# Optimization experiments

Hardware: AMD Instinct MI355X
Metric: run time of the kernel (lower is better)

Reference implementation:

```python
import jax, jax.numpy as jnp
import numpy as np

N_NODES = 100000
N_EDGES = 1600000
D_FEAT = 64


def setup_inputs() -> dict:
    key = jax.random.key(0)
    k1, k2 = jax.random.split(key)
    x = jax.random.normal(k1, (N_NODES, D_FEAT), dtype=jnp.float32)
    edge_index = jax.random.randint(k2, (2, N_EDGES), 0, N_NODES, dtype=jnp.int64)
    alpha = jnp.ones((), dtype=jnp.float32)
    res_scale = jnp.ones((), dtype=jnp.float32)
    return {"x": x, "alpha": alpha, "res_scale": res_scale, "edge_index": edge_index}


def reference(x, alpha, res_scale, edge_index):
    """LGConv (symmetric gcn_norm, no self-loops) -> alpha-scale -> residual.

    out_i = alpha * sum_{(j->i) in E} x_j / sqrt(deg_i * deg_j) + res_scale * x_i
    """
    n = x.shape[0]
    row, col = edge_index[0], edge_index[1]  # source, target
    # degree from target index (as in PyG gcn_norm with add_self_loops=False)
    deg = jax.ops.segment_sum(jnp.ones(row.shape[0], dtype=x.dtype), col, num_segments=n)
    deg_inv_sqrt = jnp.where(deg > 0, jax.lax.rsqrt(jnp.maximum(deg, 1.0)), 0.0)
    norm = deg_inv_sqrt[row] * deg_inv_sqrt[col]  # (E,)
    msgs = norm[:, None] * x[row]                  # (E, d) gather + scale
    out = jax.ops.segment_sum(msgs, col, num_segments=n)  # scatter-add to targets
    return alpha * out + res_scale * x
```

## Files before the change

kernel.cpp:

```cpp
#include <hip/hip_runtime.h>
#include <hip/hip_bf16.h>

#define D_FEAT 64
#define OVF_CAP 65536
#define EB 4096
#define NBMAX 1024

typedef unsigned int uint32;

__device__ inline float blo(uint32 u) { return __uint_as_float(u << 16); }
__device__ inline float bhi(uint32 u) { return __uint_as_float(u & 0xffff0000u); }
__device__ inline float dinv(int d) { return (d > 0) ? rsqrtf((float)d) : 0.0f; }

__global__ __launch_bounds__(1024) void k_scatter(const int* __restrict__ row,
                                                  const int* __restrict__ col,
                                                  const float2* __restrict__ x2,
                                                  uint32* __restrict__ xb,
                                                  int* __restrict__ deg,
                                                  int* __restrict__ cursor,
                                                  uint32* __restrict__ binned,
                                                  int* __restrict__ slots,
                                                  int2* __restrict__ ovf,
                                                  int* __restrict__ ovf_cnt,
                                                  int nhalf, int E, int nb,
                                                  int CAP, int C) {
    __shared__ int h[NBMAX];
    for (int i = threadIdx.x; i < nb; i += 1024) h[i] = 0;
    __syncthreads();
    const int s = blockIdx.x * EB;
    const int e = (s + EB < E) ? s + EB : E;
    for (int i = s + threadIdx.x; i < e; i += 1024)
        atomicAdd(&h[col[i] >> 7], 1);
    __syncthreads();
    for (int k = threadIdx.x; k < nb; k += 1024) {
        int c = h[k];
        if (c) h[k] = atomicAdd(&cursor[k], c);
    }
    __syncthreads();
    for (int i = s + threadIdx.x; i < e; i += 1024) {
        int c = col[i];
        uint32 r = (uint32)row[i];
        int b = c >> 7;
        int pos = atomicAdd(&h[b], 1);
        if (pos < CAP) {
            binned[(size_t)b * CAP + pos] = (r << 7) | (uint32)(c & 127);
        } else {
            int rk = atomicAdd(&deg[c], 1);
            if (rk < C) {
                slots[(size_t)c * C + rk] = (int)r;
            } else {
                int o = atomicAdd(ovf_cnt, 1);
                if (o < OVF_CAP) ovf[o] = make_int2((int)r, c);
            }
        }
    }
    const int t = blockIdx.x * 1024 + threadIdx.x;
    const int stride = gridDim.x * 1024;
    for (int j = t; j < nhalf; j += stride) {
        float2 v = x2[j];
        __hip_bfloat16 bx = __float2bfloat16(v.x);
        __hip_bfloat16 by = __float2bfloat16(v.y);
        uint32 ux = *reinterpret_cast<unsigned short*>(&bx);
        uint32 uy = *reinterpret_cast<unsigned short*>(&by);
        xb[j] = ux | (uy << 16);
    }
}

__global__ __launch_bounds__(512) void k_build(const int* __restrict__ cursor,
                                               const uint32* __restrict__ binned,
                                               int* __restrict__ slots,
                                               int* __restrict__ deg,
                                               float* __restrict__ winv,
                                               int2* __restrict__ ovf,
                                               int* __restrict__ ovf_cnt,
                                               int n, int C, int CAP) {
    __shared__ int cnt[128];
    const int k = blockIdx.x;
    const int base = k << 7;
    if (threadIdx.x < 128) {
        int node = base + threadIdx.x;
        cnt[threadIdx.x] = (node < n) ? deg[node] : 0;
    }
    __syncthreads();
    int tot = cursor[k];
    const int e = (tot < CAP) ? tot : CAP;
    const uint32* seg = binned + (size_t)k * CAP;
    for (int i = threadIdx.x; i < e; i += 512) {
        uint32 pk = seg[i];
        int cl = (int)(pk & 127);
        int r  = (int)(pk >> 7);
        int rk = atomicAdd(&cnt[cl], 1);
        if (rk < C) {
            slots[(size_t)(base + cl) * C + rk] = r;
        } else {
            int o = atomicAdd(ovf_cnt, 1);
            if (o < OVF_CAP) ovf[o] = make_int2(r, base + cl);
        }
    }
    __syncthreads();
    int i = base + threadIdx.x;
    if (threadIdx.x < 128 && i < n) {
        int d = cnt[threadIdx.x];
        deg[i] = d;
        winv[i] = dinv(d);
    }
}

__global__ void k_gather4d(const uint32* __restrict__ xb,
                           const float4* __restrict__ x4,
                           const int* __restrict__ deg,
                           const float* __restrict__ winv,
                           const int* __restrict__ slots,
                           const float* __restrict__ alpha_p,
                           const float* __restrict__ rs_p,
                           float4* __restrict__ out4, int n, int C) {
    int wid = (blockIdx.x * blockDim.x + threadIdx.x) >> 6;
    if (wid >= n) return;
    const int lane = threadIdx.x & 63;
    const int q = lane >> 4;
    const int l = lane & 15;
    int d = deg[wid];
    int e = (d < C) ? d : C;
    float4 xr = make_float4(0.f, 0.f, 0.f, 0.f);
    if (q == 0) xr = x4[(size_t)wid * 16 + l];
    const int* sl = slots + (size_t)wid * C;
    float ax = 0.f, ay = 0.f, az = 0.f, aw = 0.f;
    int k = 0;
    for (; k + 16 <= e; k += 16) {
        int s0 = sl[k + q];
        int s1 = sl[k + 4 + q];
        int s2 = sl[k + 8 + q];
        int s3 = sl[k + 12 + q];
        float w0 = winv[s0], w1 = winv[s1], w2 = winv[s2], w3 = winv[s3];
        uint2 p0 = ((const uint2*)(xb + (size_t)s0 * 32))[l];
        uint2 p1 = ((const uint2*)(xb + (size_t)s1 * 32))[l];
        uint2 p2 = ((const uint2*)(xb + (size_t)s2 * 32))[l];
        uint2 p3 = ((const uint2*)(xb + (size_t)s3 * 32))[l];
        ax = fmaf(w0, blo(p0.x), ax); ay = fmaf(w0, bhi(p0.x), ay);
        az = fmaf(w0, blo(p0.y), az); aw = fmaf(w0, bhi(p0.y), aw);
        ax = fmaf(w1, blo(p1.x), ax); ay = fmaf(w1, bhi(p1.x), ay);
        az = fmaf(w1, blo(p1.y), az); aw = fmaf(w1, bhi(p1.y), aw);
        ax = fmaf(w2, blo(p2.x), ax); ay = fmaf(w2, bhi(p2.x), ay);
        az = fmaf(w2, blo(p2.y), az); aw = fmaf(w2, bhi(p2.y), aw);
        ax = fmaf(w3, blo(p3.x), ax); ay = fmaf(w3, bhi(p3.x), ay);
        az = fmaf(w3, blo(p3.y), az); aw = fmaf(w3, bhi(p3.y), aw);
    }
    for (; k < e; k += 4) {
        int kk = k + q;
        if (kk < e) {
            int s0 = sl[kk];
            float w0 = winv[s0];
            uint2 p0 = ((const uint2*)(xb + (size_t)s0 * 32))[l];
            ax = fmaf(w0, blo(p0.x), ax); ay = fmaf(w0, bhi(p0.x), ay);
            az = fmaf(w0, blo(p0.y), az); aw = fmaf(w0, bhi(p0.y), aw);
        }
    }
    ax += __shfl_down(ax, 32, 64); ay += __shfl_down(ay, 32, 64);
    az += __shfl_down(az, 32, 64); aw += __shfl_down(aw, 32, 64);
    ax += __shfl_down(ax, 16, 64); ay += __shfl_down(ay, 16, 64);
    az += __shfl_down(az, 16, 64); aw += __shfl_down(aw, 16, 64);
    if (q == 0) {
        float adw = (*alpha_p) * winv[wid];
        float rs  = *rs_p;
        float4 o;
        o.x = fmaf(adw, ax, rs * xr.x);
        o.y = fmaf(adw, ay, rs * xr.y);
        o.z = fmaf(adw, az, rs * xr.z);
        o.w = fmaf(adw, aw, rs * xr.w);
        out4[(size_t)wid * 16 + l] = o;
    }
}

__global__ void k_ovf(const int2* __restrict__ ovf, const int* __restrict__ cnt_p,
                      const float* __restrict__ x, const float* __restrict__ winv,
                      const float* __restrict__ alpha_p, float* __restrict__ out) {
    int cnt = *cnt_p;
    if (cnt > OVF_CAP) cnt = OVF_CAP;
    if (cnt <= 0) return;
    float a = *alpha_p;
    long long total = (long long)cnt * 64;
    long long stride = (long long)gridDim.x * blockDim.x;
    for (long long idx = blockIdx.x * (long long)blockDim.x + threadIdx.x;
         idx < total; idx += stride) {
        int e = (int)(idx >> 6);
        int f = (int)(idx & 63);
        int2 rc = ovf[e];
        float w = a * winv[rc.x] * winv[rc.y];
        atomicAdd(&out[(size_t)rc.y * D_FEAT + f], w * x[(size_t)rc.x * D_FEAT + f]);
    }
}

__global__ void k_winv(const int* __restrict__ deg, float* __restrict__ winv, int n) {
    int i = blockIdx.x * blockDim.x + threadIdx.x;
    if (i < n) winv[i] = dinv(deg[i]);
}

__global__ __launch_bounds__(256) void k_prep(const float2* __restrict__ x2,
                                              uint32* __restrict__ xb,
                                              const int* __restrict__ row,
                                              const int* __restrict__ col,
                                              int* __restrict__ deg,
                                              int* __restrict__ slots,
                                              int2* __restrict__ ovf,
                                              int* __restrict__ ovf_cnt,
                                              int nhalf, int E, int C) {
    const int t = blockIdx.x * blockDim.x + threadIdx.x;
    if (t < E) {
        int c = col[t];
        int r = row[t];
        int rk = atomicAdd(&deg[c], 1);
        if (rk < C) {
            slots[(size_t)c * C + rk] = r;
        } else {
            int o = atomicAdd(ovf_cnt, 1);
            if (o < OVF_CAP) ovf[o] = make_int2(r, c);
        }
    }
    const int stride = gridDim.x * blockDim.x;
    for (int j = t; j < nhalf; j += stride) {
        float2 v = x2[j];
        __hip_bfloat16 bx = __float2bfloat16(v.x);
        __hip_bfloat16 by = __float2bfloat16(v.y);
        uint32 ux = *reinterpret_cast<unsigned short*>(&bx);
        uint32 uy = *reinterpret_cast<unsigned short*>(&by);
        xb[j] = ux | (uy << 16);
    }
}

static inline char* align_up(char* p, size_t a) {
    return (char*)(((uintptr_t)p + (a - 1)) & ~(uintptr_t)(a - 1));
}

extern "C" void kernel_launch(void* const* d_in, const int* in_sizes, int n_in,
                              void* d_out, int out_size, void* d_ws, size_t ws_size,
                              hipStream_t stream) {
    const float* x         = (const float*)d_in[0];
    const float* alpha     = (const float*)d_in[1];
    const float* res_scale = (const float*)d_in[2];
    const int*   ei        = (const int*)d_in[3];

    const int n = in_sizes[0] / D_FEAT;
    const int E = in_sizes[3] / 2;
    const int* row = ei;
    const int* col = ei + E;

    float* out = (float*)d_out;
    const int nhalf = n * (D_FEAT / 2);
    const int nb = (n + 127) >> 7;
    const int B  = (E + EB - 1) / EB;
    const int C  = 32;

    {
        char* p = (char*)d_ws;
        int*    deg     = (int*)p;            p += (size_t)n * 4;
        int*    cursor  = (int*)p;            p += (size_t)nb * 4;
        int*    ovf_cnt = (int*)p;            p += 4;
        float*  winv    = (float*)p;          p += (size_t)n * 4;
        int2*   ovf     = (int2*)p;           p += (size_t)OVF_CAP * 8;
        p = align_up(p, 16);
        uint32* xb      = (uint32*)p;         p += (size_t)n * 128;
        int*    slots   = (int*)p;            p += (size_t)n * C * 4;
        p = align_up(p, 16);
        uint32* binned  = (uint32*)p;
        const size_t fixed = (size_t)((char*)binned - (char*)d_ws);

        int CAP = 0;
        if (ws_size > fixed) {
            long long avail = (long long)(ws_size - fixed) / ((long long)nb * 4);
            CAP = (avail > 4096) ? 4096 : (int)avail;
            CAP &= ~31;
        }
        const bool ok = (CAP >= 1600) && (nb <= NBMAX) && (n <= (NBMAX << 7));
        if (ok) {
            hipMemsetAsync(deg, 0, (size_t)(n + nb + 1) * 4, stream);
            k_scatter<<<B, 1024, 0, stream>>>(row, col, (const float2*)x, xb,
                                              deg, cursor, binned, slots,
                                              ovf, ovf_cnt, nhalf, E, nb, CAP, C);
            k_build<<<nb, 512, 0, stream>>>(cursor, binned, slots, deg, winv,
                                            ovf, ovf_cnt, n, C, CAP);
            const long long tt = (long long)n * D_FEAT;
            const int blocks = (int)((tt + 255) / 256);
            k_gather4d<<<blocks, 256, 0, stream>>>(xb, (const float4*)x, deg, winv,
                                                   slots, alpha, res_scale,
                                                   (float4*)out, n, C);
            k_ovf<<<64, 256, 0, stream>>>(ovf, ovf_cnt, x, winv, alpha, out);
            return;
        }
    }

    {
        char* q = (char*)d_ws;
        int*    degf    = (int*)q;            q += (size_t)n * 4;
        int*    ovf_cf  = (int*)q;            q += 4;
        float*  winvf   = (float*)q;          q += (size_t)n * 4;
        int2*   ovff    = (int2*)q;           q += (size_t)OVF_CAP * 8;
        q = align_up(q, 16);
        uint32* xbf     = (uint32*)q;         q += (size_t)n * 128;
        int*    slotsf  = (int*)q;
        const size_t fxd = (size_t)(q - (char*)d_ws);
        int Cf = 0;
        if (ws_size > fxd) {
            size_t c_avail = (ws_size - fxd) / ((size_t)n * 4);
            Cf = (c_avail > 32) ? 32 : (int)c_avail;
        }
        if (Cf < 1) return;
        hipMemsetAsync(degf, 0, (size_t)n * 4 + 4, stream);
        k_prep<<<(E + 255) / 256, 256, 0, stream>>>(
            (const float2*)x, xbf, row, col, degf, slotsf, ovff, ovf_cf,
            nhalf, E, Cf);
        k_winv<<<(n + 255) / 256, 256, 0, stream>>>(degf, winvf, n);
        const long long tt = (long long)n * D_FEAT;
        const int blocks = (int)((tt + 255) / 256);
        k_gather4d<<<blocks, 256, 0, stream>>>(xbf, (const float4*)x, degf, winvf,
                                               slotsf, alpha, res_scale,
                                               (float4*)out, n, Cf);
        k_ovf<<<64, 256, 0, stream>>>(ovff, ovf_cf, x, winvf, alpha, out);
    }
}
```

Baseline: 182.4 us.

## Replace global bin cursors with per-block local counting sort and offset table

The scatter kernel now does a block-local counting sort of its edge chunk in shared memory (histogram, prefix scan, staged write) and writes a contiguous sorted chunk plus per-bin offsets. This removes the global cursor atomics and the CAP-limited bin buffers. The build kernel then walks every block's offset range for its bin, one source block per thread. This drops the atomic contention and the scattered binned writes, but adds a serial inner loop in build whose per-thread work is uneven, and a larger offset table to read.

```diff
diff --git a/kernel.cpp b/kernel.cpp
--- a/kernel.cpp
+++ b/kernel.cpp
@@ -5,6 +5,7 @@
 #define OVF_CAP 65536
 #define EB 4096
 #define NBMAX 1024
+#define CSL 32
 
 typedef unsigned int uint32;
 
@@ -12,50 +13,55 @@
 __device__ inline float bhi(uint32 u) { return __uint_as_float(u & 0xffff0000u); }
 __device__ inline float dinv(int d) { return (d > 0) ? rsqrtf((float)d) : 0.0f; }
 
-__global__ __launch_bounds__(1024) void k_scatter(const int* __restrict__ row,
-                                                  const int* __restrict__ col,
-                                                  const float2* __restrict__ x2,
-                                                  uint32* __restrict__ xb,
-                                                  int* __restrict__ deg,
-                                                  int* __restrict__ cursor,
-                                                  uint32* __restrict__ binned,
-                                                  int* __restrict__ slots,
-                                                  int2* __restrict__ ovf,
-                                                  int* __restrict__ ovf_cnt,
-                                                  int nhalf, int E, int nb,
-                                                  int CAP, int C) {
-    __shared__ int h[NBMAX];
-    for (int i = threadIdx.x; i < nb; i += 1024) h[i] = 0;
-    __syncthreads();
-    const int s = blockIdx.x * EB;
+__global__ __launch_bounds__(1024) void k_split(const int* __restrict__ row,
+                                                const int* __restrict__ col,
+                                                const float2* __restrict__ x2,
+                                                uint32* __restrict__ xb,
+                                                uint32* __restrict__ binned2,
+                                                int* __restrict__ off,
+                                                int nhalf, int E, int nb, int B) {
+    __shared__ int    h[NBMAX];
+    __shared__ int    P[1024];
+    __shared__ uint32 st[EB];
+    const int tid = threadIdx.x;
+    const int b = blockIdx.x;
+    for (int i = tid; i < nb; i += 1024) h[i] = 0;
+    __syncthreads();
+    const int s = b * EB;
     const int e = (s + EB < E) ? s + EB : E;
-    for (int i = s + threadIdx.x; i < e; i += 1024)
+    for (int i = s + tid; i < e; i += 1024)
         atomicAdd(&h[col[i] >> 7], 1);
     __syncthreads();
-    for (int k = threadIdx.x; k < nb; k += 1024) {
-        int c = h[k];
-        if (c) h[k] = atomicAdd(&cursor[k], c);
-    }
-    __syncthreads();
-    for (int i = s + threadIdx.x; i < e; i += 1024) {
+    P[tid] = (tid < nb) ? h[tid] : 0;
+    __syncthreads();
+    for (int o = 1; o < 1024; o <<= 1) {
+        int v = P[tid];
+        if (tid >= o) v += P[tid - o];
+        __syncthreads();
+        P[tid] = v;
+        __syncthreads();
+    }
+    int cntk = 0, excl = 0;
+    if (tid < nb) { cntk = h[tid]; excl = P[tid] - cntk; }
+    __syncthreads();
+    if (tid < nb) {
+        h[tid] = excl;
+        off[(size_t)b * (nb + 1) + tid] = excl;
+    }
+    if (tid == 0) off[(size_t)b * (nb + 1) + nb] = e - s;
+    __syncthreads();
+    for (int i = s + tid; i < e; i += 1024) {
         int c = col[i];
         uint32 r = (uint32)row[i];
-        int b = c >> 7;
-        int pos = atomicAdd(&h[b], 1);
-        if (pos < CAP) {
-            binned[(size_t)b * CAP + pos] = (r << 7) | (uint32)(c & 127);
-        } else {
-            int rk = atomicAdd(&deg[c], 1);
-            if (rk < C) {
-                slots[(size_t)c * C + rk] = (int)r;
-            } else {
-                int o = atomicAdd(ovf_cnt, 1);
-                if (o < OVF_CAP) ovf[o] = make_int2((int)r, c);
-            }
-        }
-    }
-    const int t = blockIdx.x * 1024 + threadIdx.x;
-    const int stride = gridDim.x * 1024;
+        int pos = atomicAdd(&h[c >> 7], 1);
+        st[pos] = (r << 7) | (uint32)(c & 127);
+    }
+    __syncthreads();
+    const int tot = e - s;
+    uint32* dst = binned2 + (size_t)b * EB;
+    for (int i = tid; i < tot; i += 1024) dst[i] = st[i];
+    const int t = b * 1024 + tid;
+    const int stride = B * 1024;
     for (int j = t; j < nhalf; j += stride) {
         float2 v = x2[j];
         __hip_bfloat16 bx = __float2bfloat16(v.x);
@@ -66,43 +72,45 @@
     }
 }
 
-__global__ __launch_bounds__(512) void k_build(const int* __restrict__ cursor,
-                                               const uint32* __restrict__ binned,
+__global__ __launch_bounds__(512) void k_build(const uint32* __restrict__ binned2,
+                                               const int* __restrict__ off,
                                                int* __restrict__ slots,
                                                int* __restrict__ deg,
                                                float* __restrict__ winv,
                                                int2* __restrict__ ovf,
                                                int* __restrict__ ovf_cnt,
-                                               int n, int C, int CAP) {
+                                               int n, int nb, int B) {
     __shared__ int cnt[128];
     const int k = blockIdx.x;
+    const int tid = threadIdx.x;
+    if (tid < 128) cnt[tid] = 0;
+    __syncthreads();
     const int base = k << 7;
-    if (threadIdx.x < 128) {
-        int node = base + threadIdx.x;
-        cnt[threadIdx.x] = (node < n) ? deg[node] : 0;
-    }
-    __syncthreads();
-    int tot = cursor[k];
-    const int e = (tot < CAP) ? tot : CAP;
-    const uint32* seg = binned + (size_t)k * CAP;
-    for (int i = threadIdx.x; i < e; i += 512) {
-        uint32 pk = seg[i];
-        int cl = (int)(pk & 127);
-        int r  = (int)(pk >> 7);
-        int rk = atomicAdd(&cnt[cl], 1);
-        if (rk < C) {
-            slots[(size_t)(base + cl) * C + rk] = r;
-        } else {
-            int o = atomicAdd(ovf_cnt, 1);
-            if (o < OVF_CAP) ovf[o] = make_int2(r, base + cl);
-        }
-    }
-    __syncthreads();
-    int i = base + threadIdx.x;
-    if (threadIdx.x < 128 && i < n) {
-        int d = cnt[threadIdx.x];
-        deg[i] = d;
-        winv[i] = dinv(d);
+    for (int b = tid; b < B; b += 512) {
+        const int* ob = off + (size_t)b * (nb + 1) + k;
+        int o0 = ob[0], o1 = ob[1];
+        const uint32* sl = binned2 + (size_t)b * EB;
+        for (int i = o0; i < o1; ++i) {
+            uint32 pk = sl[i];
+            int cl = (int)(pk & 127);
+            int r  = (int)(pk >> 7);
+            int rk = atomicAdd(&cnt[cl], 1);
+            if (rk < CSL) {
+                slots[(size_t)(base + cl) * CSL + rk] = r;
+            } else {
+                int o = atomicAdd(ovf_cnt, 1);
+                if (o < OVF_CAP) ovf[o] = make_int2(r, base + cl);
+            }
+        }
+    }
+    __syncthreads();
+    if (tid < 128) {
+        int node = base + tid;
+        if (node < n) {
+            int d = cnt[tid];
+            deg[node] = d;
+            winv[node] = dinv(d);
+        }
     }
 }
 
@@ -248,41 +256,33 @@
     const int nhalf = n * (D_FEAT / 2);
     const int nb = (n + 127) >> 7;
     const int B  = (E + EB - 1) / EB;
-    const int C  = 32;
 
     {
         char* p = (char*)d_ws;
         int*    deg     = (int*)p;            p += (size_t)n * 4;
-        int*    cursor  = (int*)p;            p += (size_t)nb * 4;
         int*    ovf_cnt = (int*)p;            p += 4;
         float*  winv    = (float*)p;          p += (size_t)n * 4;
         int2*   ovf     = (int2*)p;           p += (size_t)OVF_CAP * 8;
         p = align_up(p, 16);
         uint32* xb      = (uint32*)p;         p += (size_t)n * 128;
-        int*    slots   = (int*)p;            p += (size_t)n * C * 4;
+        int*    slots   = (int*)p;            p += (size_t)n * CSL * 4;
         p = align_up(p, 16);
-        uint32* binned  = (uint32*)p;
-        const size_t fixed = (size_t)((char*)binned - (char*)d_ws);
-
-        int CAP = 0;
-        if (ws_size > fixed) {
-            long long avail = (long long)(ws_size - fixed) / ((long long)nb * 4);
-            CAP = (avail > 4096) ? 4096 : (int)avail;
-            CAP &= ~31;
-        }
-        const bool ok = (CAP >= 1600) && (nb <= NBMAX) && (n <= (NBMAX << 7));
+        uint32* binned2 = (uint32*)p;         p += (size_t)B * EB * 4;
+        int*    off     = (int*)p;            p += (size_t)B * (nb + 1) * 4;
+        const size_t need = (size_t)(p - (char*)d_ws);
+
+        const bool ok = (need <= ws_size) && (nb <= NBMAX) && (n <= (NBMAX << 7));
         if (ok) {
-            hipMemsetAsync(deg, 0, (size_t)(n + nb + 1) * 4, stream);
-            k_scatter<<<B, 1024, 0, stream>>>(row, col, (const float2*)x, xb,
-                                              deg, cursor, binned, slots,
-                                              ovf, ovf_cnt, nhalf, E, nb, CAP, C);
-            k_build<<<nb, 512, 0, stream>>>(cursor, binned, slots, deg, winv,
-                                            ovf, ovf_cnt, n, C, CAP);
+            hipMemsetAsync(ovf_cnt, 0, 4, stream);
+            k_split<<<B, 1024, 0, stream>>>(row, col, (const float2*)x, xb,
+                                            binned2, off, nhalf, E, nb, B);
+            k_build<<<nb, 512, 0, stream>>>(binned2, off, slots, deg, winv,
+                                            ovf, ovf_cnt, n, nb, B);
             const long long tt = (long long)n * D_FEAT;
             const int blocks = (int)((tt + 255) / 256);
             k_gather4d<<<blocks, 256, 0, stream>>>(xb, (const float4*)x, deg, winv,
                                                    slots, alpha, res_scale,
-                                                   (float4*)out, n, C);
+                                                   (float4*)out, n, CSL);
             k_ovf<<<64, 256, 0, stream>>>(ovf, ovf_cnt, x, winv, alpha, out);
             return;
         }
```

After: 190.9 us. 4.6% more time.
